# Optimization experiments

Measured on AMD Instinct MI355X. Metric: run time of the kernel, lower is better.

The kernel has to match this reference:

```python
import jax, jax.numpy as jnp
import numpy as np

POOLING_COUNTS = [15, 8, 8, 8]
N = 128


def _build_entries():
    """Replicates SparseMaxPool.__init__: per step (kernel, pool_stride, i_idx, j_idx)."""
    entries = []
    stride, offset = 1, 0
    for ci, c in enumerate(POOLING_COUNTS):
        for k in range(c):
            offset += stride
            # pooler layout: first block all MaxPool1d(2,1); later blocks start with MaxPool1d(3,2)
            kernel = 3 if (ci > 0 and k == 0) else 2
            pstride = 2 if kernel == 3 else 1
            i = np.arange(0, N - offset, stride)
            j = np.arange(offset, N, stride)
            entries.append((kernel, pstride, i, j))
        stride *= 2
    return entries

_ENTRIES = _build_entries()


def _maxpool1d(x, kernel, stride):
    # x: [B, D, L] -> [B, D, (L-kernel)//stride + 1]
    L = x.shape[-1]
    out = (L - kernel) // stride + 1
    slices = [x[..., t : t + (out - 1) * stride + 1 : stride] for t in range(kernel)]
    y = slices[0]
    for s in slices[1:]:
        y = jnp.maximum(y, s)
    return y


def setup_inputs() -> dict:
    key = jax.random.key(0)
    x = jax.random.normal(key, (16, 256, N), dtype=jnp.float32)
    return {"x": x}


def reference(x):
    B, D, Nv = x.shape
    map2d = jnp.zeros((B, D, N, N), dtype=x.dtype)
    diag = np.arange(N)
    map2d = map2d.at[:, :, diag, diag].set(x)
    for kernel, pstride, i, j in _ENTRIES:
        x = _maxpool1d(x, kernel, pstride)
        map2d = map2d.at[:, :, i, j].set(x)
    return map2d
```

## Files before the change

kernel.cpp:

```cpp
#include <hip/hip_runtime.h>


#define NN 128
#define SLICE_ELEMS (NN * NN)
#define VOFF 784
#define NVAL 2560
#define ZERO_SLOT (VOFF + NVAL)
#define LDS_WORDS (VOFF + NVAL + 1)
#define NBUILD 2560
#define NODESC 16384

__device__ __forceinline__ void seg_params(int s, int& o, int& sh) {
    if (s < 16)      { o = s;                sh = 0; }
    else if (s < 24) { o = 17 + 2 * (s - 16); sh = 1; }
    else if (s < 32) { o = 35 + 4 * (s - 24); sh = 2; }
    else             { o = 71 + 8 * (s - 32); sh = 3; }
}

__global__ __launch_bounds__(256) void sp_init(unsigned int* __restrict__ bdesc,
                                               unsigned short* __restrict__ odesc) {
    int idx = blockIdx.x * 256 + threadIdx.x;
    if (idx < NODESC) {
        int r = idx >> 7, c = idx & 127;
        int o = c - r;
        int sh = -1, s = 0;
        if (o >= 0 && o <= 15)                          { sh = 0; s = o; }
        else if (o >= 17 && o <= 31 && (o & 1) == 1)    { sh = 1; s = 16 + ((o - 17) >> 1); }
        else if (o >= 35 && o <= 63 && (o & 3) == 3)    { sh = 2; s = 24 + ((o - 35) >> 2); }
        else if (o >= 71 && o <= 127 && (o & 7) == 7)   { sh = 3; s = 32 + ((o - 71) >> 3); }
        unsigned short addr = (unsigned short)ZERO_SLOT;
        if (sh >= 0 && (r & ((1 << sh) - 1)) == 0) {
            int base = 0;
            for (int t = 0; t < s; ++t) {
                int oo, ss; seg_params(t, oo, ss);
                base += ((127 - oo) >> ss) + 1;
            }
            addr = (unsigned short)(VOFF + base + (r >> sh));
        }
        odesc[idx] = addr;
    } else if (idx < NODESC + NBUILD) {
        int i = idx - NODESC;
        unsigned int desc = 0;
        int base = 0;
        for (int t = 0; t < 40; ++t) {
            int oo, ss; seg_params(t, oo, ss);
            int cnt = ((127 - oo) >> ss) + 1;
            if (i < base + cnt) {
                int r = (i - base) << ss;
                int w = oo + 1;
                int k = 31 - __clz(w);
                int p2 = 1 << k;
                int lb = 129 * k - (p2 - 1);
                int s1 = lb + r;
                int s2 = lb + r + (w - p2);
                desc = (unsigned)s1 | ((unsigned)s2 << 16);
                break;
            }
            base += cnt;
        }
        bdesc[i] = desc;
    }
}

__global__ __launch_bounds__(256) void sp_main(const float* __restrict__ x,
                                               float* __restrict__ out,
                                               const unsigned int* __restrict__ bdesc,
                                               const unsigned short* __restrict__ odesc) {
    __shared__ float buf[LDS_WORDS];
    const int tid = threadIdx.x;
    const int slice = blockIdx.x;

    if (tid < NN) buf[tid] = x[(size_t)slice * NN + tid];
    if (tid == 255) buf[ZERO_SLOT] = 0.0f;
    __syncthreads();

    int base_prev = 0, base_cur = NN;
    #pragma unroll
    for (int k = 1; k <= 7; ++k) {
        int half = 1 << (k - 1);
        int len = (NN + 1) - (1 << k);
        if (tid < len)
            buf[base_cur + tid] = fmaxf(buf[base_prev + tid], buf[base_prev + tid + half]);
        __syncthreads();
        base_prev = base_cur;
        base_cur += len;
    }

    #pragma unroll
    for (int it = 0; it < NBUILD / 256; ++it) {
        int i = it * 256 + tid;
        unsigned int d = bdesc[i];
        buf[VOFF + i] = fmaxf(buf[d & 0xffff], buf[d >> 16]);
    }
    __syncthreads();

    float4* __restrict__ out_s = reinterpret_cast<float4*>(out + (size_t)slice * SLICE_ELEMS);
    const uint2* __restrict__ od = reinterpret_cast<const uint2*>(odesc);
    #pragma unroll
    for (int it = 0; it < 16; ++it) {
        int idx = it * 256 + tid;
        uint2 d = od[idx];
        float4 v;
        v.x = buf[d.x & 0xffff];
        v.y = buf[d.x >> 16];
        v.z = buf[d.y & 0xffff];
        v.w = buf[d.y >> 16];
        out_s[idx] = v;
    }
}

extern "C" void kernel_launch(void* const* d_in, const int* in_sizes, int n_in,
                              void* d_out, int out_size, void* d_ws, size_t ws_size,
                              hipStream_t stream) {
    const float* x = (const float*)d_in[0];
    float* out = (float*)d_out;
    unsigned int* bdesc = (unsigned int*)d_ws;
    unsigned short* odesc = (unsigned short*)((char*)d_ws + NBUILD * 4);

    const int init_items = NODESC + NBUILD;
    sp_init<<<dim3((init_items + 255) / 256), dim3(256), 0, stream>>>(bdesc, odesc);

    const int slices = in_sizes[0] / NN;
    sp_main<<<dim3(slices), dim3(256), 0, stream>>>(x, out, bdesc, odesc);
}
```

Measured before the change: 260.2 us.

## Re-layout LDS pooled values by column to cut bank conflicts in output gather

Pooled values in LDS are now stored at addresses keyed by output column and segment instead of packed sequentially. The goal is that lanes gathering adjacent output columns read different LDS banks. The single zero slot becomes 32 column-indexed zero slots. The build descriptors are repacked to hold source, offset delta and destination address. The price is a larger LDS footprint and a more complex descriptor encoding with tight bit-field limits.

```diff
diff --git a/kernel.cpp b/kernel.cpp
--- a/kernel.cpp
+++ b/kernel.cpp
@@ -3,18 +3,22 @@
 
 #define NN 128
 #define SLICE_ELEMS (NN * NN)
-#define VOFF 784
-#define NVAL 2560
-#define ZERO_SLOT (VOFF + NVAL)
-#define LDS_WORDS (VOFF + NVAL + 1)
+#define VOFF2 800
+#define ZBASE 5920
+#define SCRATCH 5952
+#define LDS_WORDS 5956
 #define NBUILD 2560
 #define NODESC 16384
 
 __device__ __forceinline__ void seg_params(int s, int& o, int& sh) {
-    if (s < 16)      { o = s;                sh = 0; }
+    if (s < 16)      { o = s;                 sh = 0; }
     else if (s < 24) { o = 17 + 2 * (s - 16); sh = 1; }
     else if (s < 32) { o = 35 + 4 * (s - 24); sh = 2; }
     else             { o = 71 + 8 * (s - 32); sh = 3; }
+}
+
+__device__ __forceinline__ int val_addr(int c, int s) {
+    return VOFF2 + (c >> 2) + (((c & 3) * 40 + s) << 5);
 }
 
 __global__ __launch_bounds__(256) void sp_init(unsigned int* __restrict__ bdesc,
@@ -24,36 +28,32 @@
         int r = idx >> 7, c = idx & 127;
         int o = c - r;
         int sh = -1, s = 0;
-        if (o >= 0 && o <= 15)                          { sh = 0; s = o; }
-        else if (o >= 17 && o <= 31 && (o & 1) == 1)    { sh = 1; s = 16 + ((o - 17) >> 1); }
-        else if (o >= 35 && o <= 63 && (o & 3) == 3)    { sh = 2; s = 24 + ((o - 35) >> 2); }
-        else if (o >= 71 && o <= 127 && (o & 7) == 7)   { sh = 3; s = 32 + ((o - 71) >> 3); }
-        unsigned short addr = (unsigned short)ZERO_SLOT;
-        if (sh >= 0 && (r & ((1 << sh) - 1)) == 0) {
-            int base = 0;
-            for (int t = 0; t < s; ++t) {
-                int oo, ss; seg_params(t, oo, ss);
-                base += ((127 - oo) >> ss) + 1;
-            }
-            addr = (unsigned short)(VOFF + base + (r >> sh));
-        }
+        if (o >= 0 && o <= 15)                         { sh = 0; s = o; }
+        else if (o >= 17 && o <= 31 && (o & 1) == 1)   { sh = 1; s = 16 + ((o - 17) >> 1); }
+        else if (o >= 35 && o <= 63 && (o & 3) == 3)   { sh = 2; s = 24 + ((o - 35) >> 2); }
+        else if (o >= 71 && o <= 127 && (o & 7) == 7)  { sh = 3; s = 32 + ((o - 71) >> 3); }
+        unsigned short addr = (unsigned short)(ZBASE + (c >> 2));
+        if (sh >= 0 && (r & ((1 << sh) - 1)) == 0)
+            addr = (unsigned short)val_addr(c, s);
         odesc[idx] = addr;
     } else if (idx < NODESC + NBUILD) {
         int i = idx - NODESC;
-        unsigned int desc = 0;
+        unsigned int desc = (unsigned)SCRATCH << 16;
         int base = 0;
         for (int t = 0; t < 40; ++t) {
             int oo, ss; seg_params(t, oo, ss);
             int cnt = ((127 - oo) >> ss) + 1;
             if (i < base + cnt) {
                 int r = (i - base) << ss;
+                int c = r + oo;
                 int w = oo + 1;
                 int k = 31 - __clz(w);
                 int p2 = 1 << k;
                 int lb = 129 * k - (p2 - 1);
                 int s1 = lb + r;
-                int s2 = lb + r + (w - p2);
-                desc = (unsigned)s1 | ((unsigned)s2 << 16);
+                int d2 = w - p2;
+                int dest = val_addr(c, t);
+                desc = (unsigned)s1 | ((unsigned)d2 << 10) | ((unsigned)dest << 16);
                 break;
             }
             base += cnt;
@@ -71,7 +71,7 @@
     const int slice = blockIdx.x;
 
     if (tid < NN) buf[tid] = x[(size_t)slice * NN + tid];
-    if (tid == 255) buf[ZERO_SLOT] = 0.0f;
+    else if (tid >= 128 && tid < 160) buf[ZBASE + (tid - 128)] = 0.0f;
     __syncthreads();
 
     int base_prev = 0, base_cur = NN;
@@ -90,7 +90,10 @@
     for (int it = 0; it < NBUILD / 256; ++it) {
         int i = it * 256 + tid;
         unsigned int d = bdesc[i];
-        buf[VOFF + i] = fmaxf(buf[d & 0xffff], buf[d >> 16]);
+        int s1 = d & 1023;
+        int d2 = (d >> 10) & 63;
+        int dest = d >> 16;
+        buf[dest] = fmaxf(buf[s1], buf[s1 + d2]);
     }
     __syncthreads();
 
```

Result: no change. 262.0 us (+0.7%).
